# Kernel tuning notes

Hardware: AMD Instinct MI355X
Metric: run time of the kernel (lower is better)

The kernel has to match this reference:

```python
import jax, jax.numpy as jnp
import numpy as np

D_MODEL = 512
NUM_HEADS = 8
HEAD_DIM = D_MODEL // NUM_HEADS


def setup_inputs() -> dict:
    key = jax.random.key(0)
    ks = jax.random.split(key, 12)
    B, S, D = 4, 2048, D_MODEL
    s = 1.0 / np.sqrt(D)
    return {
        "x": jax.random.normal(ks[0], (B, S, D), dtype=jnp.float32),
        "timestamps": jax.random.uniform(ks[1], (B, S), dtype=jnp.float32),
        "attention_mask": jnp.ones((B, S), dtype=jnp.int32),
        "Wq": jax.random.normal(ks[2], (D, D), dtype=jnp.float32) * s,
        "bq": jnp.zeros((D,), dtype=jnp.float32),
        "Wk": jax.random.normal(ks[3], (D, D), dtype=jnp.float32) * s,
        "bk": jnp.zeros((D,), dtype=jnp.float32),
        "Wv": jax.random.normal(ks[4], (D, D), dtype=jnp.float32) * s,
        "bv": jnp.zeros((D,), dtype=jnp.float32),
        "Wo": jax.random.normal(ks[5], (D, D), dtype=jnp.float32) * s,
        "bo": jnp.zeros((D,), dtype=jnp.float32),
        "decay_lambda": jnp.ones((NUM_HEADS,), dtype=jnp.float32),
    }


def reference(x, timestamps, attention_mask, Wq, bq, Wk, bk, Wv, bv, Wo, bo, decay_lambda):
    B, S, D = x.shape
    H, hd = NUM_HEADS, HEAD_DIM
    scale = hd ** -0.5
    q = (x @ Wq + bq).reshape(B, S, H, hd)
    k = (x @ Wk + bk).reshape(B, S, H, hd)
    v = (x @ Wv + bv).reshape(B, S, H, hd)
    # [B,H,S,S] raw scores
    scores = jnp.einsum("bihd,bjhd->bhij", q, k) * scale
    # learnable exponential time decay, multiplied into scores
    time_diff_abs = jnp.abs(timestamps[:, :, None] - timestamps[:, None, :])  # [B,S,S]
    lam = jax.nn.softplus(decay_lambda)  # [H]
    decay_bias = jnp.exp(-lam[None, :, None, None] * time_diff_abs[:, None])  # [B,H,S,S]
    scores = scores * decay_bias
    # mask over key positions
    scores = jnp.where(attention_mask[:, None, None, :] == 0, -jnp.inf, scores)
    attn = jax.nn.softmax(scores, axis=-1)
    out = jnp.einsum("bhij,bjhd->bihd", attn, v).reshape(B, S, D)
    out = out @ Wo + bo
    return out, attn
```

## Files before the change

### kernel.cpp

```cpp
#include <hip/hip_runtime.h>


#define S_LEN  2048
#define DM     512
#define NH     8
#define HDIM   64
#define BATCH  4
#define BHN    32
#define BSROWS 8192

typedef __attribute__((ext_vector_type(8))) short short8v;
typedef __attribute__((ext_vector_type(8))) unsigned short ushort8v;
typedef __attribute__((ext_vector_type(4))) unsigned short ushort4v;
typedef __attribute__((ext_vector_type(4))) float f32x4;
typedef __attribute__((ext_vector_type(2))) unsigned int uint2v;

static __device__ __forceinline__ unsigned short bf16_rne(float f){
  unsigned int u = __float_as_uint(f);
  u = (u + 0x7FFFu + ((u >> 16) & 1u)) >> 16;
  return (unsigned short)u;
}
static __device__ __forceinline__ float bf16_f32(unsigned short h){
  return __uint_as_float(((unsigned int)h) << 16);
}
static __device__ __forceinline__ unsigned int pack2bf(float a, float b){
  return (unsigned int)bf16_rne(a) | ((unsigned int)bf16_rne(b) << 16);
}
static __device__ __forceinline__ f32x4 mfma16(short8v a, short8v b, f32x4 c){
  return __builtin_amdgcn_mfma_f32_16x16x32_bf16(a, b, c, 0, 0, 0);
}
static __device__ __forceinline__ void gll16(const unsigned short* g, unsigned short* l){
  __builtin_amdgcn_global_load_lds(
      (const __attribute__((address_space(1))) unsigned int*)g,
      (__attribute__((address_space(3))) unsigned int*)l, 16, 0, 0);
}

__global__ void k_split(const float* __restrict__ src,
                        unsigned short* __restrict__ hi,
                        unsigned short* __restrict__ lo, int n){
  for (int i = blockIdx.x*blockDim.x + threadIdx.x; i < n;
       i += gridDim.x*blockDim.x){
    float f = src[i];
    unsigned short h = bf16_rne(f);
    hi[i] = h;
    lo[i] = bf16_rne(f - bf16_f32(h));
  }
}

__global__ void k_wsplit4(
    const float* __restrict__ Wq, const float* __restrict__ Wk,
    const float* __restrict__ Wv, const float* __restrict__ Wo,
    unsigned short* __restrict__ qh, unsigned short* __restrict__ ql,
    unsigned short* __restrict__ kh, unsigned short* __restrict__ kl,
    unsigned short* __restrict__ vh, unsigned short* __restrict__ vl,
    unsigned short* __restrict__ oh, unsigned short* __restrict__ ol)
{
  int idx = blockIdx.x*blockDim.x + threadIdx.x;
  int wsel = idx >> 18;
  int off  = idx & 262143;
  int n = off >> 9, k = off & 511;
  const float* W = wsel==0 ? Wq : wsel==1 ? Wk : wsel==2 ? Wv : Wo;
  unsigned short* H = wsel==0 ? qh : wsel==1 ? kh : wsel==2 ? vh : oh;
  unsigned short* L = wsel==0 ? ql : wsel==1 ? kl : wsel==2 ? vl : ol;
  float f = W[k*DM + n];
  unsigned short h = bf16_rne(f);
  H[off] = h;
  L[off] = bf16_rne(f - bf16_f32(h));
}

__global__ __launch_bounds__(256, 3) void k_gemm_split(
    const unsigned short* __restrict__ Ahi, const unsigned short* __restrict__ Alo,
    const unsigned short* __restrict__ BThi, const unsigned short* __restrict__ BTlo,
    const float* __restrict__ bias,
    float* __restrict__ outF,
    unsigned short* __restrict__ outHi, unsigned short* __restrict__ outLo,
    int M, int N, int K, int mode, float cscale)
{
  __shared__ __align__(16) unsigned short At[2][2][128][32];
  __shared__ __align__(16) unsigned short Bt[2][2][64][32];
  const int lane = threadIdx.x & 63, w = threadIdx.x >> 6;
  const int lr = lane & 15, lk = lane >> 4;
  const int rowbase = blockIdx.y*128;
  const int colbase = blockIdx.x*64;
  const int wrow = (w >> 1)*64;
  const int wcol = (w & 1)*32;

  const int srow = w*16 + (lane>>2);
  const int ssw  = ((lane&3) ^ ((lane>>3)&3))*8;
  const unsigned short* asrc_h = Ahi + (size_t)(rowbase + srow)*K + ssw;
  const unsigned short* asrc_l = Alo + (size_t)(rowbase + srow)*K + ssw;
  const unsigned short* bsrc_h = BThi + (size_t)(colbase + srow)*K + ssw;
  const unsigned short* bsrc_l = BTlo + (size_t)(colbase + srow)*K + ssw;
  unsigned short* adst_h = &At[0][0][w*16][0];
  unsigned short* adst_l = &At[0][1][w*16][0];
  unsigned short* bdst_h = &Bt[0][0][w*16][0];
  unsigned short* bdst_l = &Bt[0][1][w*16][0];

#define GSTAGE(KS, BB) { \
    int k0_ = (KS)*32; \
    gll16(asrc_h + k0_,                adst_h + (BB)*8192); \
    gll16(asrc_h + (size_t)64*K + k0_, adst_h + (BB)*8192 + 2048); \
    gll16(asrc_l + k0_,                adst_l + (BB)*8192); \
    gll16(asrc_l + (size_t)64*K + k0_, adst_l + (BB)*8192 + 2048); \
    gll16(bsrc_h + k0_,                bdst_h + (BB)*4096); \
    gll16(bsrc_l + k0_,                bdst_l + (BB)*4096); }

  const int csw = (lk ^ ((lr>>1)&3))*8;
  const unsigned short* Ard_h = &At[0][0][wrow + lr][0] + csw;
  const unsigned short* Ard_l = &At[0][1][wrow + lr][0] + csw;
  const unsigned short* Brd_h = &Bt[0][0][wcol + lr][0] + csw;
  const unsigned short* Brd_l = &Bt[0][1][wcol + lr][0] + csw;

  f32x4 acc[4][2];
#pragma unroll
  for (int mi=0; mi<4; ++mi)
#pragma unroll
    for (int ni=0; ni<2; ++ni) acc[mi][ni] = (f32x4){0.f,0.f,0.f,0.f};

  GSTAGE(0, 0);
  __syncthreads();

  const int NKS = K >> 5;
  for (int ks = 0; ks < NKS; ++ks){
    const int c = ks & 1;
    if (ks + 1 < NKS) GSTAGE(ks+1, c^1);
    short8v ah[4], al[4], bhf[2], blf[2];
#pragma unroll
    for (int mi=0; mi<4; ++mi){
      ah[mi] = *(const short8v*)(Ard_h + c*8192 + mi*512);
      al[mi] = *(const short8v*)(Ard_l + c*8192 + mi*512);
    }
#pragma unroll
    for (int ni=0; ni<2; ++ni){
      bhf[ni] = *(const short8v*)(Brd_h + c*4096 + ni*512);
      blf[ni] = *(const short8v*)(Brd_l + c*4096 + ni*512);
    }
#pragma unroll
    for (int mi=0; mi<4; ++mi)
#pragma unroll
      for (int ni=0; ni<2; ++ni){
        acc[mi][ni] = mfma16(ah[mi], blf[ni], acc[mi][ni]);
        acc[mi][ni] = mfma16(al[mi], bhf[ni], acc[mi][ni]);
        acc[mi][ni] = mfma16(ah[mi], bhf[ni], acc[mi][ni]);
      }
    __syncthreads();
  }
#undef GSTAGE

#pragma unroll
  for (int mi=0; mi<4; ++mi)
#pragma unroll
    for (int ni=0; ni<2; ++ni){
      const int col = colbase + wcol + ni*16 + lr;
      const int row0 = rowbase + wrow + mi*16 + lk*4;
      if (mode == 1){
        int b = row0 >> 11, s0 = row0 & 2047, hh = col >> 6, d = col & 63;
        ushort4v t;
#pragma unroll
        for (int r=0;r<4;++r)
          t[r] = bf16_rne((acc[mi][ni][r] + bias[col]) * cscale);
        *(ushort4v*)(outHi + ((size_t)(b*NH + hh)*HDIM + d)*S_LEN + s0) = t;
      } else {
#pragma unroll
        for (int r=0;r<4;++r){
          int row = row0 + r;
          float cvl = (acc[mi][ni][r] + bias[col]) * cscale;
          if (mode == 2){
            outF[(size_t)row*N + col] = cvl;
          } else {
            int b = row >> 11, s = row & 2047, hh = col >> 6, d = col & 63;
            size_t off = (((size_t)(b*NH + hh))*S_LEN + s)*HDIM + d;
            unsigned short hb = bf16_rne(cvl);
            outHi[off] = hb;
            outLo[off] = bf16_rne(cvl - bf16_f32(hb));
          }
        }
      }
    }
}

__global__ __launch_bounds__(256) void k_rowsum(
    const unsigned short* __restrict__ qhi,
    const unsigned short* __restrict__ khi,
    const float* __restrict__ ts, const int* __restrict__ am,
    const float* __restrict__ dlam,
    float* __restrict__ rs_part)
{
  __shared__ __align__(16) unsigned short K_t[2][32][64];
  __shared__ __align__(16) float ts_l[1024];
  __shared__ __align__(16) float mb_l[1024];
  const int w = threadIdx.x >> 6, lane = threadIdx.x & 63;
  const int lr = lane & 15, lk = lane >> 4;
  const int wg = blockIdx.x;
  const int sw = (wg & 7)*256 + (wg >> 3);
  const int bh = sw >> 6, rem = sw & 63, it = rem >> 1, jh = rem & 1;
  const int b = bh >> 3, h = bh & 7;
  const int i0 = it*64 + w*16;
  const int j0 = jh*1024;

  const float* tsb = ts + b*S_LEN;
  const int*   amb = am + b*S_LEN;
  for (int i = threadIdx.x; i < 1024; i += 256){
    ts_l[i] = tsb[j0+i];
    mb_l[i] = amb[j0+i] ? 0.f : -1e30f;
  }

  float nlam2 = -log1pf(expf(dlam[h])) * 1.44269504f;
  nlam2 = __uint_as_float(__builtin_amdgcn_readfirstlane(__float_as_uint(nlam2)));

  size_t qoff = ((size_t)bh*S_LEN + i0 + lr)*HDIM + lk*8;
  const short8v qh0 = *(const short8v*)(qhi + qoff);
  const short8v qh1 = *(const short8v*)(qhi + qoff + 32);
  const float ti = tsb[i0 + lr];

  const unsigned short* kbh = khi + ((size_t)bh*S_LEN + j0)*HDIM;
  const unsigned short* ksrc = kbh + ((lane>>3))*64
                             + (((lane&7)^((lane>>3)&7))*8) + w*512;
  unsigned short* kdst = &K_t[0][0][0] + w*512;

  gll16(ksrc, kdst);
  __syncthreads();

  float rs = 0.f;
  for (int t = 0; t < 32; ++t){
    const int c = t & 1;
    if (t < 31) gll16(ksrc + (t+1)*2048, kdst + (c^1)*2048);
#pragma unroll
    for (int s = 0; s < 2; ++s){
      const unsigned short* Kr = &K_t[c][s*16 + lr][0];
      short8v a0 = *(const short8v*)(Kr + ((lk ^ (lr&7))*8));
      short8v a1 = *(const short8v*)(Kr + (((4+lk) ^ (lr&7))*8));
      f32x4 sA = (f32x4){0.f,0.f,0.f,0.f};
      sA = mfma16(a0, qh0, sA);
      sA = mfma16(a1, qh1, sA);
      const int jb = t*32 + s*16 + lk*4;
      f32x4 ts4 = *(const f32x4*)&ts_l[jb];
      f32x4 mb4 = *(const f32x4*)&mb_l[jb];
#pragma unroll
      for (int r=0;r<4;++r){
        float dec = __builtin_amdgcn_exp2f(nlam2 * fabsf(ti - ts4[r]));
        rs += __builtin_amdgcn_exp2f(__builtin_fmaf(sA[r], dec, mb4[r]));
      }
    }
    __syncthreads();
  }
  rs += __shfl_xor(rs, 16, 64);
  rs += __shfl_xor(rs, 32, 64);
  if (lane < 16)
    rs_part[(size_t)(jh*BHN + bh)*S_LEN + i0 + lane] = rs;
}

__global__ __launch_bounds__(256, 4) void k_pass2(
    const unsigned short* __restrict__ qhi, const unsigned short* __restrict__ qlo,
    const unsigned short* __restrict__ khi, const unsigned short* __restrict__ klo,
    const unsigned short* __restrict__ vT,
    const float* __restrict__ ts, const int* __restrict__ am,
    const float* __restrict__ dlam,
    const float* __restrict__ rs_part,
    float* __restrict__ attn,
    unsigned short* __restrict__ p0hi, unsigned short* __restrict__ p0lo,
    unsigned short* __restrict__ p1hi, unsigned short* __restrict__ p1lo)
{
  __shared__ __align__(16) unsigned short K_t[2][2][32][64];
  __shared__ __align__(16) unsigned short V_t[2][64][32];
  __shared__ __align__(16) float ts_l[1024];
  __shared__ __align__(16) float mb_l[1024];
  __shared__ __align__(16) unsigned int pb[4][16][20];
  const int w = threadIdx.x >> 6, lane = threadIdx.x & 63;
  const int lr = lane & 15, lk = lane >> 4;
  const int wg = blockIdx.x;
  const int sw = (wg & 7)*256 + (wg >> 3);
  const int bh = sw >> 6, rem = sw & 63, it = rem >> 1, jh = rem & 1;
  const int b = bh >> 3, h = bh & 7;
  const int i0 = it*64 + w*16;
  const int j0 = jh*1024;

  const float* tsb = ts + b*S_LEN;
  const int*   amb = am + b*S_LEN;
  for (int i = threadIdx.x; i < 1024; i += 256){
    ts_l[i] = tsb[j0+i];
    mb_l[i] = amb[j0+i] ? 0.f : -1e30f;
  }

  float nlam2 = -log1pf(expf(dlam[h])) * 1.44269504f;
  nlam2 = __uint_as_float(__builtin_amdgcn_readfirstlane(__float_as_uint(nlam2)));

  size_t qoff = ((size_t)bh*S_LEN + i0 + lr)*HDIM + lk*8;
  const short8v qh0 = *(const short8v*)(qhi + qoff);
  const short8v qh1 = *(const short8v*)(qhi + qoff + 32);
  const short8v ql0 = *(const short8v*)(qlo + qoff);
  const short8v ql1 = *(const short8v*)(qlo + qoff + 32);
  const float ti = tsb[i0 + lr];

  float tot = rs_part[(size_t)bh*S_LEN + i0 + lr]
            + rs_part[(size_t)(BHN + bh)*S_LEN + i0 + lr];
  const float rinv = tot > 0.f ? 1.f/tot : 0.f;

  const unsigned short* kbh = khi + ((size_t)bh*S_LEN + j0)*HDIM;
  const unsigned short* kbl = klo + ((size_t)bh*S_LEN + j0)*HDIM;
  const unsigned short* vtb = vT + (size_t)bh*HDIM*S_LEN;
  unsigned int* pbw = &pb[w][0][0];

  const int ksw = ((lane&7)^((lane>>3)&7))*8;
  const unsigned short* ksrc_h = kbh + (lane>>3)*64 + ksw + w*512;
  const unsigned short* ksrc_l = kbl + (lane>>3)*64 + ksw + w*512;
  const unsigned short* vsrc = vtb + ((size_t)(w*16 + (lane>>2)))*S_LEN + j0
                             + (((lane&3)^((lane>>4)&3))*8);
  unsigned short* kdst_h = &K_t[0][0][0][0] + w*512;
  unsigned short* kdst_l = &K_t[0][1][0][0] + w*512;
  unsigned short* vdst   = &V_t[0][0][0]    + w*512;

  const unsigned int abase = (unsigned int)(bh*S_LEN + i0 + lr)*S_LEN + j0;

  gll16(ksrc_h, kdst_h);
  gll16(ksrc_l, kdst_l);
  gll16(vsrc,   vdst);
  __syncthreads();

  f32x4 oaccT0 = (f32x4){0.f,0.f,0.f,0.f};
  f32x4 oaccT1 = (f32x4){0.f,0.f,0.f,0.f};
  f32x4 oaccT2 = (f32x4){0.f,0.f,0.f,0.f};
  f32x4 oaccT3 = (f32x4){0.f,0.f,0.f,0.f};

  for (int t = 0; t < 32; ++t){
    const int c = t & 1;
    if (t < 31){
      gll16(ksrc_h + (t+1)*2048, kdst_h + (c^1)*4096);
      gll16(ksrc_l + (t+1)*2048, kdst_l + (c^1)*4096);
      gll16(vsrc   + (t+1)*32,   vdst   + (c^1)*2048);
    }
#pragma unroll
    for (int s = 0; s < 2; ++s){
      const unsigned short* Kr0 = &K_t[c][0][s*16 + lr][0];
      const unsigned short* Kr1 = &K_t[c][1][s*16 + lr][0];
      short8v kh0 = *(const short8v*)(Kr0 + ((lk ^ (lr&7))*8));
      short8v kh1 = *(const short8v*)(Kr0 + (((4+lk) ^ (lr&7))*8));
      short8v kl0 = *(const short8v*)(Kr1 + ((lk ^ (lr&7))*8));
      short8v kl1 = *(const short8v*)(Kr1 + (((4+lk) ^ (lr&7))*8));
      f32x4 s1 = (f32x4){0.f,0.f,0.f,0.f};
      s1 = mfma16(kh0, ql0, s1);
      s1 = mfma16(kl0, qh0, s1);
      s1 = mfma16(kh1, ql1, s1);
      s1 = mfma16(kl1, qh1, s1);
      f32x4 s2 = (f32x4){0.f,0.f,0.f,0.f};
      s2 = mfma16(kh0, qh0, s2);
      s2 = mfma16(kh1, qh1, s2);
      const int jb = t*32 + s*16 + lk*4;
      f32x4 ts4 = *(const f32x4*)&ts_l[jb];
      f32x4 mb4 = *(const f32x4*)&mb_l[jb];
      f32x4 pv;
#pragma unroll
      for (int r=0;r<4;++r){
        float sa = s1[r] + s2[r];
        float dec = __builtin_amdgcn_exp2f(nlam2 * fabsf(ti - ts4[r]));
        float e = __builtin_amdgcn_exp2f(__builtin_fmaf(sa, dec, mb4[r]));
        pv[r] = e * rinv;
      }
      *(f32x4*)(attn + abase + jb) = pv;
      uint2v pk; pk.x = pack2bf(pv[0], pv[1]); pk.y = pack2bf(pv[2], pv[3]);
      *(uint2v*)&pbw[lr*20 + s*8 + 2*lk] = pk;
    }
    short8v pa = *(const short8v*)&pbw[lr*20 + 4*lk];
    const int vsw = (lr>>2)&3;
    short8v vf0 = *(const short8v*)&V_t[c][ 0 + lr][(lk ^ vsw)*8];
    short8v vf1 = *(const short8v*)&V_t[c][16 + lr][(lk ^ vsw)*8];
    short8v vf2 = *(const short8v*)&V_t[c][32 + lr][(lk ^ vsw)*8];
    short8v vf3 = *(const short8v*)&V_t[c][48 + lr][(lk ^ vsw)*8];
    oaccT0 = mfma16(vf0, pa, oaccT0);
    oaccT1 = mfma16(vf1, pa, oaccT1);
    oaccT2 = mfma16(vf2, pa, oaccT2);
    oaccT3 = mfma16(vf3, pa, oaccT3);
    asm volatile("s_waitcnt vmcnt(2) lgkmcnt(0)" ::: "memory");
    __builtin_amdgcn_s_barrier();
  }

  unsigned short* phi = jh ? p1hi : p0hi;
  unsigned short* plo = jh ? p1lo : p0lo;
  const size_t rowb = (size_t)(b*S_LEN + i0 + lr)*DM + h*HDIM + lk*4;
  float oa[4][4] = {
    {oaccT0[0],oaccT0[1],oaccT0[2],oaccT0[3]},
    {oaccT1[0],oaccT1[1],oaccT1[2],oaccT1[3]},
    {oaccT2[0],oaccT2[1],oaccT2[2],oaccT2[3]},
    {oaccT3[0],oaccT3[1],oaccT3[2],oaccT3[3]}};
#pragma unroll
  for (int nt=0;nt<4;++nt){
    ushort4v hh, ll;
#pragma unroll
    for (int r=0;r<4;++r){
      float vv = oa[nt][r];
      unsigned short hb = bf16_rne(vv);
      hh[r] = hb;
      ll[r] = bf16_rne(vv - bf16_f32(hb));
    }
    *(ushort4v*)(phi + rowb + nt*16) = hh;
    *(ushort4v*)(plo + rowb + nt*16) = ll;
  }
}

__global__ __launch_bounds__(256) void k_combine(
    const unsigned short* __restrict__ h1, const unsigned short* __restrict__ l1,
    unsigned short* __restrict__ oh, unsigned short* __restrict__ ol, int n8)
{
  int i = blockIdx.x*blockDim.x + threadIdx.x;
  if (i >= n8) return;
  size_t base = (size_t)i*8;
  ushort8v a = *(const ushort8v*)(oh + base);
  ushort8v bq = *(const ushort8v*)(ol + base);
  ushort8v c = *(const ushort8v*)(h1 + base);
  ushort8v d = *(const ushort8v*)(l1 + base);
  ushort8v rh, rl;
#pragma unroll
  for (int j=0;j<8;++j){
    float f = bf16_f32(a[j]) + bf16_f32(bq[j]) + bf16_f32(c[j]) + bf16_f32(d[j]);
    unsigned short hb = bf16_rne(f);
    rh[j] = hb;
    rl[j] = bf16_rne(f - bf16_f32(hb));
  }
  *(ushort8v*)(oh + base) = rh;
  *(ushort8v*)(ol + base) = rl;
}

extern "C" void kernel_launch(void* const* d_in, const int* in_sizes, int n_in,
                              void* d_out, int out_size, void* d_ws, size_t ws_size,
                              hipStream_t stream){
  const float* x  = (const float*)d_in[0];
  const float* ts = (const float*)d_in[1];
  const int*   am = (const int*)d_in[2];
  const float* Wq = (const float*)d_in[3];
  const float* bq = (const float*)d_in[4];
  const float* Wk = (const float*)d_in[5];
  const float* bk = (const float*)d_in[6];
  const float* Wv = (const float*)d_in[7];
  const float* bv = (const float*)d_in[8];
  const float* Wo = (const float*)d_in[9];
  const float* bo = (const float*)d_in[10];
  const float* dl = (const float*)d_in[11];

  char* ws = (char*)d_ws;
  unsigned short* xhi = (unsigned short*)(ws);
  unsigned short* xlo = (unsigned short*)(ws + 8388608ull);
  unsigned short* wqt_hi = (unsigned short*)(ws + 16777216ull + 0ull*524288ull);
  unsigned short* wqt_lo = (unsigned short*)(ws + 16777216ull + 1ull*524288ull);
  unsigned short* wkt_hi = (unsigned short*)(ws + 16777216ull + 2ull*524288ull);
  unsigned short* wkt_lo = (unsigned short*)(ws + 16777216ull + 3ull*524288ull);
  unsigned short* wvt_hi = (unsigned short*)(ws + 16777216ull + 4ull*524288ull);
  unsigned short* wvt_lo = (unsigned short*)(ws + 16777216ull + 5ull*524288ull);
  unsigned short* wot_hi = (unsigned short*)(ws + 16777216ull + 6ull*524288ull);
  unsigned short* wot_lo = (unsigned short*)(ws + 16777216ull + 7ull*524288ull);
  unsigned short* qhi = (unsigned short*)(ws + 20971520ull + 0ull*8388608ull);
  unsigned short* qlo = (unsigned short*)(ws + 20971520ull + 1ull*8388608ull);
  unsigned short* khi = (unsigned short*)(ws + 20971520ull + 2ull*8388608ull);
  unsigned short* klo = (unsigned short*)(ws + 20971520ull + 3ull*8388608ull);
  unsigned short* vt  = (unsigned short*)(ws + 20971520ull + 4ull*8388608ull);
  float* rs_part = (float*)(ws + 16777216ull);

  float* outp  = (float*)d_out;
  float* attnp = outp + (size_t)BSROWS*DM;
  unsigned short* p1hi = (unsigned short*)d_out;
  unsigned short* p1lo = p1hi + 4194304ull;

  k_split<<<4096, 256, 0, stream>>>(x, xhi, xlo, BSROWS*DM);
  k_wsplit4<<<4096, 256, 0, stream>>>(Wq, Wk, Wv, Wo,
                                      wqt_hi, wqt_lo, wkt_hi, wkt_lo,
                                      wvt_hi, wvt_lo, wot_hi, wot_lo);

  dim3 pg(DM/64, BSROWS/128);
  k_gemm_split<<<pg, 256, 0, stream>>>(xhi, xlo, wqt_hi, wqt_lo, bq,
                                       nullptr, qhi, qlo, BSROWS, DM, DM, 0,
                                       0.18033688f);
  k_gemm_split<<<pg, 256, 0, stream>>>(xhi, xlo, wkt_hi, wkt_lo, bk,
                                       nullptr, khi, klo, BSROWS, DM, DM, 0, 1.f);
  k_gemm_split<<<pg, 256, 0, stream>>>(xhi, xlo, wvt_hi, wvt_lo, bv,
                                       nullptr, vt, nullptr, BSROWS, DM, DM, 1, 1.f);

  k_rowsum<<<2048, 256, 0, stream>>>(qhi, khi, ts, am, dl, rs_part);
  k_pass2<<<2048, 256, 0, stream>>>(qhi, qlo, khi, klo, vt, ts, am, dl,
                                    rs_part, attnp, xhi, xlo, p1hi, p1lo);
  k_combine<<<2048, 256, 0, stream>>>(p1hi, p1lo, xhi, xlo, 524288);
  k_gemm_split<<<pg, 256, 0, stream>>>(xhi, xlo, wot_hi, wot_lo, bo,
                                       outp, nullptr, nullptr, BSROWS, DM, DM, 2, 1.f);

  (void)in_sizes; (void)n_in; (void)out_size; (void)ws_size;
}
```

Baseline: 393.1 us.

## Fuse QKV projections into one GEMM and drop key-split in attention passes

Concatenates the Q, K and V weight splits so a single GEMM launch computes all three projections, with the epilogue choosing the output layout by column segment. The rowsum and pass2 kernels now loop over the full 2048-key range per workgroup instead of splitting keys in halves, which removes the partial rowsum sum and the separate combine kernel along with its extra read and write traffic. The trade-off is half as many workgroups in the attention passes, with longer serial loops per workgroup, so there is less parallelism to hide latency. pass2's launch bound also drops to 3 to make room for the larger LDS arrays.

Measured after the change: 412.9 us. +5.0%, slower.

```diff
diff --git a/kernel.cpp b/kernel.cpp
--- a/kernel.cpp
+++ b/kernel.cpp
@@ -50,32 +50,32 @@
 __global__ void k_wsplit4(
     const float* __restrict__ Wq, const float* __restrict__ Wk,
     const float* __restrict__ Wv, const float* __restrict__ Wo,
-    unsigned short* __restrict__ qh, unsigned short* __restrict__ ql,
-    unsigned short* __restrict__ kh, unsigned short* __restrict__ kl,
-    unsigned short* __restrict__ vh, unsigned short* __restrict__ vl,
-    unsigned short* __restrict__ oh, unsigned short* __restrict__ ol)
+    unsigned short* __restrict__ qkvh, unsigned short* __restrict__ qkvl,
+    unsigned short* __restrict__ oh,   unsigned short* __restrict__ ol)
 {
   int idx = blockIdx.x*blockDim.x + threadIdx.x;
   int wsel = idx >> 18;
   int off  = idx & 262143;
   int n = off >> 9, k = off & 511;
   const float* W = wsel==0 ? Wq : wsel==1 ? Wk : wsel==2 ? Wv : Wo;
-  unsigned short* H = wsel==0 ? qh : wsel==1 ? kh : wsel==2 ? vh : oh;
-  unsigned short* L = wsel==0 ? ql : wsel==1 ? kl : wsel==2 ? vl : ol;
+  unsigned short* H = (wsel<3) ? (qkvh + (size_t)wsel*262144) : oh;
+  unsigned short* L = (wsel<3) ? (qkvl + (size_t)wsel*262144) : ol;
   float f = W[k*DM + n];
   unsigned short h = bf16_rne(f);
   H[off] = h;
   L[off] = bf16_rne(f - bf16_f32(h));
 }
 
-__global__ __launch_bounds__(256, 3) void k_gemm_split(
+__global__ __launch_bounds__(256, 3) void k_gemm_qkv(
     const unsigned short* __restrict__ Ahi, const unsigned short* __restrict__ Alo,
     const unsigned short* __restrict__ BThi, const unsigned short* __restrict__ BTlo,
-    const float* __restrict__ bias,
-    float* __restrict__ outF,
-    unsigned short* __restrict__ outHi, unsigned short* __restrict__ outLo,
-    int M, int N, int K, int mode, float cscale)
+    const float* __restrict__ bq, const float* __restrict__ bk,
+    const float* __restrict__ bv,
+    unsigned short* __restrict__ qhi, unsigned short* __restrict__ qlo,
+    unsigned short* __restrict__ khi, unsigned short* __restrict__ klo,
+    unsigned short* __restrict__ vt)
 {
+  const int K = DM;
   __shared__ __align__(16) unsigned short At[2][2][128][32];
   __shared__ __align__(16) unsigned short Bt[2][2][64][32];
   const int lane = threadIdx.x & 63, w = threadIdx.x >> 6;
@@ -147,35 +147,124 @@
   }
 #undef GSTAGE
 
+  const int seg = colbase >> 9;
+#pragma unroll
+  for (int mi=0; mi<4; ++mi)
+#pragma unroll
+    for (int ni=0; ni<2; ++ni){
+      const int col = colbase + wcol + ni*16 + lr;
+      const int c2  = col & 511;
+      const int row0 = rowbase + wrow + mi*16 + lk*4;
+      const int b = row0 >> 11, s0 = row0 & 2047, hh = c2 >> 6, d = c2 & 63;
+      if (seg == 2){
+        float bias = bv[c2];
+        ushort4v t;
+#pragma unroll
+        for (int r=0;r<4;++r) t[r] = bf16_rne(acc[mi][ni][r] + bias);
+        *(ushort4v*)(vt + ((size_t)(b*NH + hh)*HDIM + d)*S_LEN + s0) = t;
+      } else {
+        const float bias = seg ? bk[c2] : bq[c2];
+        const float scl  = seg ? 1.f : 0.18033688f;
+        unsigned short* oh = seg ? khi : qhi;
+        unsigned short* ol = seg ? klo : qlo;
+#pragma unroll
+        for (int r=0;r<4;++r){
+          float cvl = (acc[mi][ni][r] + bias) * scl;
+          size_t off = (((size_t)(b*NH + hh))*S_LEN + s0 + r)*HDIM + d;
+          unsigned short hb = bf16_rne(cvl);
+          oh[off] = hb;
+          ol[off] = bf16_rne(cvl - bf16_f32(hb));
+        }
+      }
+    }
+}
+
+__global__ __launch_bounds__(256, 3) void k_gemm_out(
+    const unsigned short* __restrict__ Ahi, const unsigned short* __restrict__ Alo,
+    const unsigned short* __restrict__ BThi, const unsigned short* __restrict__ BTlo,
+    const float* __restrict__ bias, float* __restrict__ outF)
+{
+  const int K = DM, N = DM;
+  __shared__ __align__(16) unsigned short At[2][2][128][32];
+  __shared__ __align__(16) unsigned short Bt[2][2][64][32];
+  const int lane = threadIdx.x & 63, w = threadIdx.x >> 6;
+  const int lr = lane & 15, lk = lane >> 4;
+  const int rowbase = blockIdx.y*128;
+  const int colbase = blockIdx.x*64;
+  const int wrow = (w >> 1)*64;
+  const int wcol = (w & 1)*32;
+
+  const int srow = w*16 + (lane>>2);
+  const int ssw  = ((lane&3) ^ ((lane>>3)&3))*8;
+  const unsigned short* asrc_h = Ahi + (size_t)(rowbase + srow)*K + ssw;
+  const unsigned short* asrc_l = Alo + (size_t)(rowbase + srow)*K + ssw;
+  const unsigned short* bsrc_h = BThi + (size_t)(colbase + srow)*K + ssw;
+  const unsigned short* bsrc_l = BTlo + (size_t)(colbase + srow)*K + ssw;
+  unsigned short* adst_h = &At[0][0][w*16][0];
+  unsigned short* adst_l = &At[0][1][w*16][0];
+  unsigned short* bdst_h = &Bt[0][0][w*16][0];
+  unsigned short* bdst_l = &Bt[0][1][w*16][0];
+
+#define GSTAGE(KS, BB) { \
+    int k0_ = (KS)*32; \
+    gll16(asrc_h + k0_,                adst_h + (BB)*8192); \
+    gll16(asrc_h + (size_t)64*K + k0_, adst_h + (BB)*8192 + 2048); \
+    gll16(asrc_l + k0_,                adst_l + (BB)*8192); \
+    gll16(asrc_l + (size_t)64*K + k0_, adst_l + (BB)*8192 + 2048); \
+    gll16(bsrc_h + k0_,                bdst_h + (BB)*4096); \
+    gll16(bsrc_l + k0_,                bdst_l + (BB)*4096); }
+
+  const int csw = (lk ^ ((lr>>1)&3))*8;
+  const unsigned short* Ard_h = &At[0][0][wrow + lr][0] + csw;
+  const unsigned short* Ard_l = &At[0][1][wrow + lr][0] + csw;
+  const unsigned short* Brd_h = &Bt[0][0][wcol + lr][0] + csw;
+  const unsigned short* Brd_l = &Bt[0][1][wcol + lr][0] + csw;
+
+  f32x4 acc[4][2];
+#pragma unroll
+  for (int mi=0; mi<4; ++mi)
+#pragma unroll
+    for (int ni=0; ni<2; ++ni) acc[mi][ni] = (f32x4){0.f,0.f,0.f,0.f};
+
+  GSTAGE(0, 0);
+  __syncthreads();
+
+  const int NKS = K >> 5;
+  for (int ks = 0; ks < NKS; ++ks){
+    const int c = ks & 1;
+    if (ks + 1 < NKS) GSTAGE(ks+1, c^1);
+    short8v ah[4], al[4], bhf[2], blf[2];
+#pragma unroll
+    for (int mi=0; mi<4; ++mi){
+      ah[mi] = *(const short8v*)(Ard_h + c*8192 + mi*512);
+      al[mi] = *(const short8v*)(Ard_l + c*8192 + mi*512);
+    }
+#pragma unroll
+    for (int ni=0; ni<2; ++ni){
+      bhf[ni] = *(const short8v*)(Brd_h + c*4096 + ni*512);
+      blf[ni] = *(const short8v*)(Brd_l + c*4096 + ni*512);
+    }
+#pragma unroll
+    for (int mi=0; mi<4; ++mi)
+#pragma unroll
+      for (int ni=0; ni<2; ++ni){
+        acc[mi][ni] = mfma16(ah[mi], blf[ni], acc[mi][ni]);
+        acc[mi][ni] = mfma16(al[mi], bhf[ni], acc[mi][ni]);
+        acc[mi][ni] = mfma16(ah[mi], bhf[ni], acc[mi][ni]);
+      }
+    __syncthreads();
+  }
+#undef GSTAGE
+
 #pragma unroll
   for (int mi=0; mi<4; ++mi)
 #pragma unroll
     for (int ni=0; ni<2; ++ni){
       const int col = colbase + wcol + ni*16 + lr;
       const int row0 = rowbase + wrow + mi*16 + lk*4;
-      if (mode == 1){
-        int b = row0 >> 11, s0 = row0 & 2047, hh = col >> 6, d = col & 63;
-        ushort4v t;
-#pragma unroll
-        for (int r=0;r<4;++r)
-          t[r] = bf16_rne((acc[mi][ni][r] + bias[col]) * cscale);
-        *(ushort4v*)(outHi + ((size_t)(b*NH + hh)*HDIM + d)*S_LEN + s0) = t;
-      } else {
-#pragma unroll
-        for (int r=0;r<4;++r){
-          int row = row0 + r;
-          float cvl = (acc[mi][ni][r] + bias[col]) * cscale;
-          if (mode == 2){
-            outF[(size_t)row*N + col] = cvl;
-          } else {
-            int b = row >> 11, s = row & 2047, hh = col >> 6, d = col & 63;
-            size_t off = (((size_t)(b*NH + hh))*S_LEN + s)*HDIM + d;
-            unsigned short hb = bf16_rne(cvl);
-            outHi[off] = hb;
-            outLo[off] = bf16_rne(cvl - bf16_f32(hb));
-          }
-        }
-      }
+#pragma unroll
+      for (int r=0;r<4;++r)
+        outF[(size_t)(row0 + r)*N + col] = acc[mi][ni][r] + bias[col];
     }
 }
 
@@ -187,22 +276,21 @@
     float* __restrict__ rs_part)
 {
   __shared__ __align__(16) unsigned short K_t[2][32][64];
-  __shared__ __align__(16) float ts_l[1024];
-  __shared__ __align__(16) float mb_l[1024];
+  __shared__ __align__(16) float ts_l[2048];
+  __shared__ __align__(16) float mb_l[2048];
   const int w = threadIdx.x >> 6, lane = threadIdx.x & 63;
   const int lr = lane & 15, lk = lane >> 4;
   const int wg = blockIdx.x;
-  const int sw = (wg & 7)*256 + (wg >> 3);
-  const int bh = sw >> 6, rem = sw & 63, it = rem >> 1, jh = rem & 1;
+  const int sw = (wg & 7)*128 + (wg >> 3);
+  const int bh = sw >> 5, it = sw & 31;
   const int b = bh >> 3, h = bh & 7;
   const int i0 = it*64 + w*16;
-  const int j0 = jh*1024;
 
   const float* tsb = ts + b*S_LEN;
   const int*   amb = am + b*S_LEN;
-  for (int i = threadIdx.x; i < 1024; i += 256){
-    ts_l[i] = tsb[j0+i];
-    mb_l[i] = amb[j0+i] ? 0.f : -1e30f;
+  for (int i = threadIdx.x; i < S_LEN; i += 256){
+    ts_l[i] = tsb[i];
+    mb_l[i] = amb[i] ? 0.f : -1e30f;
   }
 
   float nlam2 = -log1pf(expf(dlam[h])) * 1.44269504f;
@@ -213,7 +301,7 @@
   const short8v qh1 = *(const short8v*)(qhi + qoff + 32);
   const float ti = tsb[i0 + lr];
 
-  const unsigned short* kbh = khi + ((size_t)bh*S_LEN + j0)*HDIM;
+  const unsigned short* kbh = khi + (size_t)bh*S_LEN*HDIM;
   const unsigned short* ksrc = kbh + ((lane>>3))*64
                              + (((lane&7)^((lane>>3)&7))*8) + w*512;
   unsigned short* kdst = &K_t[0][0][0] + w*512;
@@ -222,9 +310,9 @@
   __syncthreads();
 
   float rs = 0.f;
-  for (int t = 0; t < 32; ++t){
+  for (int t = 0; t < 64; ++t){
     const int c = t & 1;
-    if (t < 31) gll16(ksrc + (t+1)*2048, kdst + (c^1)*2048);
+    if (t < 63) gll16(ksrc + (size_t)(t+1)*2048, kdst + (c^1)*2048);
 #pragma unroll
     for (int s = 0; s < 2; ++s){
       const unsigned short* Kr = &K_t[c][s*16 + lr][0];
@@ -247,10 +335,10 @@
   rs += __shfl_xor(rs, 16, 64);
   rs += __shfl_xor(rs, 32, 64);
   if (lane < 16)
-    rs_part[(size_t)(jh*BHN + bh)*S_LEN + i0 + lane] = rs;
-}
-
-__global__ __launch_bounds__(256, 4) void k_pass2(
+    rs_part[(size_t)bh*S_LEN + i0 + lane] = rs;
+}
+
+__global__ __launch_bounds__(256, 3) void k_pass2(
     const unsigned short* __restrict__ qhi, const unsigned short* __restrict__ qlo,
     const unsigned short* __restrict__ khi, const unsigned short* __restrict__ klo,
     const unsigned short* __restrict__ vT,
@@ -258,28 +346,26 @@
     const float* __restrict__ dlam,
     const float* __restrict__ rs_part,
     float* __restrict__ attn,
-    unsigned short* __restrict__ p0hi, unsigned short* __restrict__ p0lo,
-    unsigned short* __restrict__ p1hi, unsigned short* __restrict__ p1lo)
+    unsigned short* __restrict__ ohi, unsigned short* __restrict__ olo)
 {
   __shared__ __align__(16) unsigned short K_t[2][2][32][64];
   __shared__ __align__(16) unsigned short V_t[2][64][32];
-  __shared__ __align__(16) float ts_l[1024];
-  __shared__ __align__(16) float mb_l[1024];
+  __shared__ __align__(16) float ts_l[2048];
+  __shared__ __align__(16) float mb_l[2048];
   __shared__ __align__(16) unsigned int pb[4][16][20];
   const int w = threadIdx.x >> 6, lane = threadIdx.x & 63;
   const int lr = lane & 15, lk = lane >> 4;
   const int wg = blockIdx.x;
-  const int sw = (wg & 7)*256 + (wg >> 3);
-  const int bh = sw >> 6, rem = sw & 63, it = rem >> 1, jh = rem & 1;
+  const int sw = (wg & 7)*128 + (wg >> 3);
+  const int bh = sw >> 5, it = sw & 31;
   const int b = bh >> 3, h = bh & 7;
   const int i0 = it*64 + w*16;
-  const int j0 = jh*1024;
 
   const float* tsb = ts + b*S_LEN;
   const int*   amb = am + b*S_LEN;
-  for (int i = threadIdx.x; i < 1024; i += 256){
-    ts_l[i] = tsb[j0+i];
-    mb_l[i] = amb[j0+i] ? 0.f : -1e30f;
+  for (int i = threadIdx.x; i < S_LEN; i += 256){
+    ts_l[i] = tsb[i];
+    mb_l[i] = amb[i] ? 0.f : -1e30f;
   }
 
   float nlam2 = -log1pf(expf(dlam[h])) * 1.44269504f;
@@ -292,25 +378,24 @@
   const short8v ql1 = *(const short8v*)(qlo + qoff + 32);
   const float ti = tsb[i0 + lr];
 
-  float tot = rs_part[(size_t)bh*S_LEN + i0 + lr]
-            + rs_part[(size_t)(BHN + bh)*S_LEN + i0 + lr];
+  float tot = rs_part[(size_t)bh*S_LEN + i0 + lr];
   const float rinv = tot > 0.f ? 1.f/tot : 0.f;
 
-  const unsigned short* kbh = khi + ((size_t)bh*S_LEN + j0)*HDIM;
-  const unsigned short* kbl = klo + ((size_t)bh*S_LEN + j0)*HDIM;
+  const unsigned short* kbh = khi + (size_t)bh*S_LEN*HDIM;
+  const unsigned short* kbl = klo + (size_t)bh*S_LEN*HDIM;
   const unsigned short* vtb = vT + (size_t)bh*HDIM*S_LEN;
   unsigned int* pbw = &pb[w][0][0];
 
   const int ksw = ((lane&7)^((lane>>3)&7))*8;
   const unsigned short* ksrc_h = kbh + (lane>>3)*64 + ksw + w*512;
   const unsigned short* ksrc_l = kbl + (lane>>3)*64 + ksw + w*512;
-  const unsigned short* vsrc = vtb + ((size_t)(w*16 + (lane>>2)))*S_LEN + j0
+  const unsigned short* vsrc = vtb + ((size_t)(w*16 + (lane>>2)))*S_LEN
                              + (((lane&3)^((lane>>4)&3))*8);
   unsigned short* kdst_h = &K_t[0][0][0][0] + w*512;
   unsigned short* kdst_l = &K_t[0][1][0][0] + w*512;
   unsigned short* vdst   = &V_t[0][0][0]    + w*512;
 
-  const unsigned int abase = (unsigned int)(bh*S_LEN + i0 + lr)*S_LEN + j0;
+  const unsigned int abase = (unsigned int)(bh*S_LEN + i0 + lr)*S_LEN;
 
   gll16(ksrc_h, kdst_h);
   gll16(ksrc_l, kdst_l);
@@ -322,12 +407,12 @@
   f32x4 oaccT2 = (f32x4){0.f,0.f,0.f,0.f};
   f32x4 oaccT3 = (f32x4){0.f,0.f,0.f,0.f};
 
-  for (int t = 0; t < 32; ++t){
+  for (int t = 0; t < 64; ++t){
     const int c = t & 1;
-    if (t < 31){
-      gll16(ksrc_h + (t+1)*2048, kdst_h + (c^1)*4096);
-      gll16(ksrc_l + (t+1)*2048, kdst_l + (c^1)*4096);
-      gll16(vsrc   + (t+1)*32,   vdst   + (c^1)*2048);
+    if (t < 63){
+      gll16(ksrc_h + (size_t)(t+1)*2048, kdst_h + (c^1)*4096);
+      gll16(ksrc_l + (size_t)(t+1)*2048, kdst_l + (c^1)*4096);
+      gll16(vsrc   + (t+1)*32,           vdst   + (c^1)*2048);
     }
 #pragma unroll
     for (int s = 0; s < 2; ++s){
@@ -374,8 +459,6 @@
     __builtin_amdgcn_s_barrier();
   }
 
-  unsigned short* phi = jh ? p1hi : p0hi;
-  unsigned short* plo = jh ? p1lo : p0lo;
   const size_t rowb = (size_t)(b*S_LEN + i0 + lr)*DM + h*HDIM + lk*4;
   float oa[4][4] = {
     {oaccT0[0],oaccT0[1],oaccT0[2],oaccT0[3]},
@@ -392,32 +475,9 @@
       hh[r] = hb;
       ll[r] = bf16_rne(vv - bf16_f32(hb));
     }
-    *(ushort4v*)(phi + rowb + nt*16) = hh;
-    *(ushort4v*)(plo + rowb + nt*16) = ll;
-  }
-}
-
-__global__ __launch_bounds__(256) void k_combine(
-    const unsigned short* __restrict__ h1, const unsigned short* __restrict__ l1,
-    unsigned short* __restrict__ oh, unsigned short* __restrict__ ol, int n8)
-{
-  int i = blockIdx.x*blockDim.x + threadIdx.x;
-  if (i >= n8) return;
-  size_t base = (size_t)i*8;
-  ushort8v a = *(const ushort8v*)(oh + base);
-  ushort8v bq = *(const ushort8v*)(ol + base);
-  ushort8v c = *(const ushort8v*)(h1 + base);
-  ushort8v d = *(const ushort8v*)(l1 + base);
-  ushort8v rh, rl;
-#pragma unroll
-  for (int j=0;j<8;++j){
-    float f = bf16_f32(a[j]) + bf16_f32(bq[j]) + bf16_f32(c[j]) + bf16_f32(d[j]);
-    unsigned short hb = bf16_rne(f);
-    rh[j] = hb;
-    rl[j] = bf16_rne(f - bf16_f32(hb));
-  }
-  *(ushort8v*)(oh + base) = rh;
-  *(ushort8v*)(ol + base) = rl;
+    *(ushort4v*)(ohi + rowb + nt*16) = hh;
+    *(ushort4v*)(olo + rowb + nt*16) = ll;
+  }
 }
 
 extern "C" void kernel_launch(void* const* d_in, const int* in_sizes, int n_in,
@@ -439,14 +499,10 @@
   char* ws = (char*)d_ws;
   unsigned short* xhi = (unsigned short*)(ws);
   unsigned short* xlo = (unsigned short*)(ws + 8388608ull);
-  unsigned short* wqt_hi = (unsigned short*)(ws + 16777216ull + 0ull*524288ull);
-  unsigned short* wqt_lo = (unsigned short*)(ws + 16777216ull + 1ull*524288ull);
-  unsigned short* wkt_hi = (unsigned short*)(ws + 16777216ull + 2ull*524288ull);
-  unsigned short* wkt_lo = (unsigned short*)(ws + 16777216ull + 3ull*524288ull);
-  unsigned short* wvt_hi = (unsigned short*)(ws + 16777216ull + 4ull*524288ull);
-  unsigned short* wvt_lo = (unsigned short*)(ws + 16777216ull + 5ull*524288ull);
-  unsigned short* wot_hi = (unsigned short*)(ws + 16777216ull + 6ull*524288ull);
-  unsigned short* wot_lo = (unsigned short*)(ws + 16777216ull + 7ull*524288ull);
+  unsigned short* wqkv_hi = (unsigned short*)(ws + 16777216ull);
+  unsigned short* wqkv_lo = (unsigned short*)(ws + 16777216ull + 1572864ull);
+  unsigned short* wot_hi  = (unsigned short*)(ws + 16777216ull + 3145728ull);
+  unsigned short* wot_lo  = (unsigned short*)(ws + 16777216ull + 3670016ull);
   unsigned short* qhi = (unsigned short*)(ws + 20971520ull + 0ull*8388608ull);
   unsigned short* qlo = (unsigned short*)(ws + 20971520ull + 1ull*8388608ull);
   unsigned short* khi = (unsigned short*)(ws + 20971520ull + 2ull*8388608ull);
@@ -456,29 +512,19 @@
 
   float* outp  = (float*)d_out;
   float* attnp = outp + (size_t)BSROWS*DM;
-  unsigned short* p1hi = (unsigned short*)d_out;
-  unsigned short* p1lo = p1hi + 4194304ull;
 
   k_split<<<4096, 256, 0, stream>>>(x, xhi, xlo, BSROWS*DM);
   k_wsplit4<<<4096, 256, 0, stream>>>(Wq, Wk, Wv, Wo,
-                                      wqt_hi, wqt_lo, wkt_hi, wkt_lo,
-                                      wvt_hi, wvt_lo, wot_hi, wot_lo);
-
-  dim3 pg(DM/64, BSROWS/128);
-  k_gemm_split<<<pg, 256, 0, stream>>>(xhi, xlo, wqt_hi, wqt_lo, bq,
-                                       nullptr, qhi, qlo, BSROWS, DM, DM, 0,
-                                       0.18033688f);
-  k_gemm_split<<<pg, 256, 0, stream>>>(xhi, xlo, wkt_hi, wkt_lo, bk,
-                                       nullptr, khi, klo, BSROWS, DM, DM, 0, 1.f);
-  k_gemm_split<<<pg, 256, 0, stream>>>(xhi, xlo, wvt_hi, wvt_lo, bv,
-                                       nullptr, vt, nullptr, BSROWS, DM, DM, 1, 1.f);
-
-  k_rowsum<<<2048, 256, 0, stream>>>(qhi, khi, ts, am, dl, rs_part);
-  k_pass2<<<2048, 256, 0, stream>>>(qhi, qlo, khi, klo, vt, ts, am, dl,
-                                    rs_part, attnp, xhi, xlo, p1hi, p1lo);
-  k_combine<<<2048, 256, 0, stream>>>(p1hi, p1lo, xhi, xlo, 524288);
-  k_gemm_split<<<pg, 256, 0, stream>>>(xhi, xlo, wot_hi, wot_lo, bo,
-                                       outp, nullptr, nullptr, BSROWS, DM, DM, 2, 1.f);
+                                      wqkv_hi, wqkv_lo, wot_hi, wot_lo);
+
+  k_gemm_qkv<<<dim3(1536/64, BSROWS/128), 256, 0, stream>>>(
+      xhi, xlo, wqkv_hi, wqkv_lo, bq, bk, bv, qhi, qlo, khi, klo, vt);
+
+  k_rowsum<<<1024, 256, 0, stream>>>(qhi, khi, ts, am, dl, rs_part);
+  k_pass2<<<1024, 256, 0, stream>>>(qhi, qlo, khi, klo, vt, ts, am, dl,
+                                    rs_part, attnp, xhi, xlo);
+  k_gemm_out<<<dim3(DM/64, BSROWS/128), 256, 0, stream>>>(
+      xhi, xlo, wot_hi, wot_lo, bo, outp);
 
   (void)in_sizes; (void)n_in; (void)out_size; (void)ws_size;
 }
```
